# Optimization experiments

Hardware: AMD Instinct MI355X
Metric: run time of the kernel (lower is better)

Reference implementation:

```python
import jax, jax.numpy as jnp
import numpy as np

T, B, N, F = 128, 8, 32, 128
H = 256  # hidden channels
DEG = 8


def setup_inputs() -> dict:
    key = jax.random.key(0)
    ks = jax.random.split(key, 8)
    data = jax.random.normal(ks[0], (T, B, N, F), jnp.float32)
    all_ohs = jax.random.normal(ks[1], (T, B, N, 8), jnp.float32)
    n0 = B * N * T
    n1 = B * N * (T // 2)
    edge_index0 = jax.random.randint(ks[2], (2, n0 * DEG), 0, n0)
    edge_index1 = jax.random.randint(ks[3], (2, n1 * DEG), 0, n1)
    def init(k, shape, fan):
        return jax.random.normal(k, shape, jnp.float32) / np.float32(np.sqrt(fan))
    W0 = init(ks[4], (2 * F, H), 2 * F); b0 = jnp.zeros((H,), jnp.float32)
    Wc0 = init(ks[5], (H, H, 5), H * 5); bc0 = jnp.zeros((H,), jnp.float32)
    W1 = init(ks[6], (2 * H, H), 2 * H); b1 = jnp.zeros((H,), jnp.float32)
    Wc1 = init(ks[7], (H, H, 5), H * 5); bc1 = jnp.zeros((H,), jnp.float32)
    return dict(data=data, all_ohs=all_ohs,
                edge_index0=edge_index0, edge_index1=edge_index1,
                W0=W0, b0=b0, Wc0=Wc0, bc0=bc0,
                W1=W1, b1=b1, Wc1=Wc1, bc1=bc1)


def edge_conv(x, edge_index, W, b):
    # PyG EdgeConv: out_i = max_{(j->i)} relu(Linear(cat[x_i, x_j - x_i]))
    src, dst = edge_index[0], edge_index[1]
    x_i = x[dst]           # [E, C] target features
    x_j = x[src]           # [E, C] source features
    msg = jax.nn.relu(jnp.concatenate([x_i, x_j - x_i], axis=-1) @ W + b)
    out = jax.ops.segment_max(msg, dst, num_segments=x.shape[0])
    return jnp.where(jnp.isneginf(out), 0.0, out)  # empty segments -> 0 (PyG fill)


def temp_conv(x, Wc, bc):
    # x: [BN, C, L]; Conv1d(k=5, pad=2) + relu + MaxPool1d(2)
    y = jax.lax.conv_general_dilated(x, Wc, (1,), [(2, 2)],
                                     dimension_numbers=('NCH', 'OIH', 'NCH'))
    y = jax.nn.relu(y + bc[None, :, None])
    L2 = y.shape[-1] // 2
    y = y[..., : L2 * 2].reshape(y.shape[0], y.shape[1], L2, 2)
    return jnp.max(y, axis=-1)


def reference(data, all_ohs, edge_index0, edge_index1,
              W0, b0, Wc0, bc0, W1, b1, Wc1, bc1):
    # 'fast' path, context=False: all_ohs unused beyond reshape
    length = data.shape[0]
    x = data.reshape(T, B * N, F).transpose(1, 0, 2).reshape(-1, F)  # [BN*T, F]
    layers = ((edge_index0, W0, b0, Wc0, bc0),
              (edge_index1, W1, b1, Wc1, bc1))
    for ei, W, b, Wc, bc in layers:
        x = edge_conv(x, ei, W, b)                       # [BN*length, C]
        x = x.reshape(-1, length, x.shape[-1])           # [BN, length, C]
        x = x.transpose(0, 2, 1)                         # [BN, C, length]
        x = temp_conv(x, Wc, bc)                         # [BN, C, length//2]
        length = x.shape[2]
        C = x.shape[1]
        x = x.transpose(0, 2, 1).reshape(-1, C)          # [BN*length, C]
    return x
```

## Files before the change

### kernel.cpp

```cpp
#include <hip/hip_runtime.h>
#include <hip/hip_bf16.h>
#include <math.h>

#define T0 128
#define BN 256
#define Ff 128
#define Hh 256
#define NODE0 32768
#define E0 262144
#define T1 64
#define NODE1 16384
#define E1 131072
#define CAP 48

typedef __attribute__((ext_vector_type(8))) short bhalf8;
typedef __attribute__((ext_vector_type(4))) float floatx4;

__device__ __forceinline__ unsigned short f2bf(float x) {
  union { float f; unsigned u; } v; v.f = x;
  unsigned r = v.u + 0x7fff + ((v.u >> 16) & 1);
  return (unsigned short)(r >> 16);
}
__device__ __forceinline__ float bf2f(unsigned short b) {
  union { unsigned u; float f; } v; v.u = ((unsigned)b) << 16;
  return v.f;
}


__global__ void k_permb(const float* __restrict__ src, unsigned short* __restrict__ dst) {
  int idx = blockIdx.x * 256 + threadIdx.x;
  int c8 = idx & 15;
  int r  = idx >> 4;
  int t  = r & (T0 - 1);
  int bn = r >> 7;
  const float* s = src + ((size_t)t * BN + bn) * Ff + c8 * 8;
  float4 a = *(const float4*)s;
  float4 b = *(const float4*)(s + 4);
  unsigned short o[8];
  o[0] = f2bf(a.x); o[1] = f2bf(a.y); o[2] = f2bf(a.z); o[3] = f2bf(a.w);
  o[4] = f2bf(b.x); o[5] = f2bf(b.y); o[6] = f2bf(b.z); o[7] = f2bf(b.w);
  *(int4*)(dst + ((size_t)(bn * T0 + t) * Ff + c8 * 8)) = *(int4*)o;
}

__global__ void k_wb(const float* __restrict__ W, unsigned short* __restrict__ Wbot_b,
                     unsigned short* __restrict__ Wd_b, int half, int kbits) {
  int idx = blockIdx.x * 256 + threadIdx.x;
  int n = idx >> kbits;
  int k = idx & (half - 1);
  float top = W[(size_t)k * 256 + n];
  float bot = W[(size_t)(half + k) * 256 + n];
  Wbot_b[idx] = f2bf(bot);
  Wd_b[idx]   = f2bf(top - bot);
}

__global__ void k_wtb(const float* __restrict__ Wc, unsigned short* __restrict__ Wtb) {
  int idx = blockIdx.x * 256 + threadIdx.x;
  int tap = idx >> 16;
  int o = (idx >> 8) & 255;
  int i = idx & 255;
  Wtb[idx] = f2bf(Wc[((size_t)o * 256 + i) * 5 + tap]);
}


__global__ void k_fill(const int* __restrict__ srcIdx, const int* __restrict__ dstIdx,
                       int* __restrict__ cnt, int* __restrict__ slot, int E) {
  int e = blockIdx.x * 256 + threadIdx.x;
  if (e < E) {
    int d = dstIdx[e];
    int p = atomicAdd(&cnt[d], 1);
    if (p < CAP) slot[(size_t)d * CAP + p] = srcIdx[e];
  }
}

__global__ __launch_bounds__(256) void k_maxg(const unsigned short* __restrict__ Bm,
                                              const int* __restrict__ cnt,
                                              const int* __restrict__ slot,
                                              unsigned short* __restrict__ Mm) {
  int node = blockIdx.x * 4 + (threadIdx.x >> 6);
  int lane = threadIdx.x & 63;
  int n = cnt[node];
  if (n > CAP) n = CAP;
  const int* sl = slot + (size_t)node * CAP;
  float4 m = make_float4(-INFINITY, -INFINITY, -INFINITY, -INFINITY);
  int i = 0;
  for (; i + 4 <= n; i += 4) {
    int s0 = sl[i], s1 = sl[i + 1], s2 = sl[i + 2], s3 = sl[i + 3];
    ushort4 v0 = *(const ushort4*)(Bm + (size_t)s0 * 256 + lane * 4);
    ushort4 v1 = *(const ushort4*)(Bm + (size_t)s1 * 256 + lane * 4);
    ushort4 v2 = *(const ushort4*)(Bm + (size_t)s2 * 256 + lane * 4);
    ushort4 v3 = *(const ushort4*)(Bm + (size_t)s3 * 256 + lane * 4);
    m.x = fmaxf(fmaxf(fmaxf(m.x, bf2f(v0.x)), fmaxf(bf2f(v1.x), bf2f(v2.x))), bf2f(v3.x));
    m.y = fmaxf(fmaxf(fmaxf(m.y, bf2f(v0.y)), fmaxf(bf2f(v1.y), bf2f(v2.y))), bf2f(v3.y));
    m.z = fmaxf(fmaxf(fmaxf(m.z, bf2f(v0.z)), fmaxf(bf2f(v1.z), bf2f(v2.z))), bf2f(v3.z));
    m.w = fmaxf(fmaxf(fmaxf(m.w, bf2f(v0.w)), fmaxf(bf2f(v1.w), bf2f(v2.w))), bf2f(v3.w));
  }
  for (; i < n; ++i) {
    int s = sl[i];
    ushort4 v = *(const ushort4*)(Bm + (size_t)s * 256 + lane * 4);
    m.x = fmaxf(m.x, bf2f(v.x));
    m.y = fmaxf(m.y, bf2f(v.y));
    m.z = fmaxf(m.z, bf2f(v.z));
    m.w = fmaxf(m.w, bf2f(v.w));
  }
  ushort4 o;
  o.x = f2bf(m.x); o.y = f2bf(m.y); o.z = f2bf(m.z); o.w = f2bf(m.w);
  *(ushort4*)(Mm + (size_t)node * 256 + lane * 4) = o;
}

template <int MODE>
__global__ __launch_bounds__(256) void k_gemm(const unsigned short* __restrict__ A,
                                              const unsigned short* __restrict__ Wb,
                                              unsigned short* __restrict__ C, int K,
                                              const float* __restrict__ bias,
                                              const unsigned short* __restrict__ Mm) {
  __shared__ __align__(16) short A_lds[128 * 72];
  __shared__ __align__(16) short B_lds[128 * 72];
  int tid = threadIdx.x;
  int row0 = blockIdx.x * 128;
  int col0 = blockIdx.y * 128;
  int lane = tid & 63, wv = tid >> 6;
  int m16 = lane & 15, quad = lane >> 4;

  floatx4 acc[2][8];
#pragma unroll
  for (int mt = 0; mt < 2; ++mt)
#pragma unroll
    for (int nt = 0; nt < 8; ++nt) acc[mt][nt] = (floatx4){0.f, 0.f, 0.f, 0.f};

  for (int kb = 0; kb < K; kb += 64) {
    __syncthreads();
#pragma unroll
    for (int i = 0; i < 4; ++i) {
      int u = tid + i * 256;
      int r = u >> 3, seg = u & 7;
      *(int4*)&A_lds[r * 72 + seg * 8] =
          *(const int4*)(A + (size_t)(row0 + r) * K + kb + seg * 8);
      *(int4*)&B_lds[r * 72 + seg * 8] =
          *(const int4*)(Wb + (size_t)(col0 + r) * K + kb + seg * 8);
    }
    __syncthreads();
#pragma unroll
    for (int ks = 0; ks < 2; ++ks) {
      bhalf8 a[2];
#pragma unroll
      for (int mt = 0; mt < 2; ++mt)
        a[mt] = *(const bhalf8*)&A_lds[(wv * 32 + mt * 16 + m16) * 72 + ks * 32 + quad * 8];
#pragma unroll
      for (int nt = 0; nt < 8; ++nt) {
        bhalf8 b = *(const bhalf8*)&B_lds[(nt * 16 + m16) * 72 + ks * 32 + quad * 8];
#pragma unroll
        for (int mt = 0; mt < 2; ++mt)
          acc[mt][nt] = __builtin_amdgcn_mfma_f32_16x16x32_bf16(a[mt], b, acc[mt][nt], 0, 0, 0);
      }
    }
  }

#pragma unroll
  for (int mt = 0; mt < 2; ++mt) {
    int g0 = row0 + wv * 32 + mt * 16 + quad * 4;
#pragma unroll
    for (int nt = 0; nt < 8; ++nt) {
      int c = col0 + nt * 16 + m16;
      float bv = (MODE == 1) ? bias[c] : 0.f;
#pragma unroll
      for (int r = 0; r < 4; ++r) {
        float v = acc[mt][nt][r];
        if (MODE == 1) v = fmaxf(v + bv + bf2f(Mm[(size_t)(g0 + r) * 256 + c]), 0.f);
        C[(size_t)(g0 + r) * 256 + c] = f2bf(v);
      }
    }
  }
}

template <int TR, bool OUT_F32>
__global__ __launch_bounds__(256) void k_conv(const unsigned short* __restrict__ X,
                                              const unsigned short* __restrict__ Wtb,
                                              const float* __restrict__ bc,
                                              void* __restrict__ Yout) {
  const int MT = TR / 64;
  __shared__ __align__(16) short A_lds[(TR + 4) * 72];
  __shared__ __align__(16) short B_lds[128 * 72];
  int tid = threadIdx.x;
  int row0 = blockIdx.x * TR;
  int col0 = blockIdx.y * 128;
  int lane = tid & 63, wv = tid >> 6;
  int m16 = lane & 15, quad = lane >> 4;

  floatx4 acc[MT][8];
#pragma unroll
  for (int mt = 0; mt < MT; ++mt)
#pragma unroll
    for (int nt = 0; nt < 8; ++nt) acc[mt][nt] = (floatx4){0.f, 0.f, 0.f, 0.f};

  for (int kb = 0; kb < 256; kb += 64) {
    __syncthreads();
    for (int u = tid; u < (TR + 4) * 8; u += 256) {
      int r = u >> 3, seg = u & 7;
      int tt = r - 2;
      int4 v = {0, 0, 0, 0};
      if (tt >= 0 && tt < TR)
        v = *(const int4*)(X + (size_t)(row0 + tt) * 256 + kb + seg * 8);
      *(int4*)&A_lds[r * 72 + seg * 8] = v;
    }
    for (int tap = 0; tap < 5; ++tap) {
      if (tap > 0) __syncthreads();
      const unsigned short* Wk = Wtb + (size_t)tap * 65536;
#pragma unroll
      for (int i = 0; i < 4; ++i) {
        int u = tid + i * 256;
        int r = u >> 3, seg = u & 7;
        *(int4*)&B_lds[r * 72 + seg * 8] =
            *(const int4*)(Wk + (size_t)(col0 + r) * 256 + kb + seg * 8);
      }
      __syncthreads();
#pragma unroll
      for (int ks = 0; ks < 2; ++ks) {
        bhalf8 a[MT];
#pragma unroll
        for (int mt = 0; mt < MT; ++mt)
          a[mt] = *(const bhalf8*)&A_lds[(wv * (16 * MT) + mt * 16 + m16 + tap) * 72 + ks * 32 + quad * 8];
#pragma unroll
        for (int nt = 0; nt < 8; ++nt) {
          bhalf8 b = *(const bhalf8*)&B_lds[(nt * 16 + m16) * 72 + ks * 32 + quad * 8];
#pragma unroll
          for (int mt = 0; mt < MT; ++mt)
            acc[mt][nt] = __builtin_amdgcn_mfma_f32_16x16x32_bf16(a[mt], b, acc[mt][nt], 0, 0, 0);
        }
      }
    }
  }

#pragma unroll
  for (int mt = 0; mt < MT; ++mt) {
    int gbase = row0 + wv * (16 * MT) + mt * 16 + quad * 4;
#pragma unroll
    for (int nt = 0; nt < 8; ++nt) {
      int c = col0 + nt * 16 + m16;
      float bv = bc[c];
      float y0 = fmaxf(acc[mt][nt][0] + bv, 0.f);
      float y1 = fmaxf(acc[mt][nt][1] + bv, 0.f);
      float y2 = fmaxf(acc[mt][nt][2] + bv, 0.f);
      float y3 = fmaxf(acc[mt][nt][3] + bv, 0.f);
      float p0 = fmaxf(y0, y1);
      float p1 = fmaxf(y2, y3);
      int o0 = gbase >> 1;
      if (OUT_F32) {
        float* Y = (float*)Yout;
        Y[(size_t)o0 * 256 + c] = p0;
        Y[(size_t)(o0 + 1) * 256 + c] = p1;
      } else {
        unsigned short* Y = (unsigned short*)Yout;
        Y[(size_t)o0 * 256 + c] = f2bf(p0);
        Y[(size_t)(o0 + 1) * 256 + c] = f2bf(p1);
      }
    }
  }
}

extern "C" void kernel_launch(void* const* d_in, const int* in_sizes, int n_in,
                              void* d_out, int out_size, void* d_ws, size_t ws_size,
                              hipStream_t stream) {
  const float* data = (const float*)d_in[0];
  const int* ei0 = (const int*)d_in[2];
  const int* ei1 = (const int*)d_in[3];
  const float* W0  = (const float*)d_in[4];
  const float* b0  = (const float*)d_in[5];
  const float* Wc0 = (const float*)d_in[6];
  const float* bc0 = (const float*)d_in[7];
  const float* W1  = (const float*)d_in[8];
  const float* b1  = (const float*)d_in[9];
  const float* Wc1 = (const float*)d_in[10];
  const float* bc1 = (const float*)d_in[11];
  float* out = (float*)d_out;

  char* base = (char*)d_ws;
  size_t off = 0;
  auto alloc = [&](size_t bytes) { void* p = base + off; off += (bytes + 255) & ~(size_t)255; return p; };
  unsigned short* X0b   = (unsigned short*)alloc((size_t)NODE0 * Ff * 2);
  unsigned short* Bm    = (unsigned short*)alloc((size_t)NODE0 * Hh * 2);
  unsigned short* Mm    = (unsigned short*)alloc((size_t)NODE0 * Hh * 2);
  unsigned short* X1b   = (unsigned short*)alloc((size_t)NODE0 * Hh * 2);
  unsigned short* Y0b   = (unsigned short*)alloc((size_t)NODE1 * Hh * 2);
  unsigned short* Wbot0 = (unsigned short*)alloc(256 * 128 * 2);
  unsigned short* Wd0   = (unsigned short*)alloc(256 * 128 * 2);
  unsigned short* Wbot1 = (unsigned short*)alloc(256 * 256 * 2);
  unsigned short* Wd1   = (unsigned short*)alloc(256 * 256 * 2);
  unsigned short* Wtb0  = (unsigned short*)alloc(5 * 65536 * 2);
  unsigned short* Wtb1  = (unsigned short*)alloc(5 * 65536 * 2);
  int* cnt0  = (int*)alloc(NODE0 * 4);
  int* cnt1  = (int*)alloc(NODE1 * 4);
  int* slot0 = (int*)alloc((size_t)NODE0 * CAP * 4);
  int* slot1 = (int*)alloc((size_t)NODE1 * CAP * 4);

  hipMemsetAsync(cnt0, 0, NODE0 * sizeof(int), stream);
  hipMemsetAsync(cnt1, 0, NODE1 * sizeof(int), stream);

  k_permb<<<NODE0 * 16 / 256, 256, 0, stream>>>(data, X0b);
  k_wb<<<256 * 128 / 256, 256, 0, stream>>>(W0, Wbot0, Wd0, 128, 7);
  k_wb<<<256 * 256 / 256, 256, 0, stream>>>(W1, Wbot1, Wd1, 256, 8);
  k_wtb<<<5 * 65536 / 256, 256, 0, stream>>>(Wc0, Wtb0);
  k_wtb<<<5 * 65536 / 256, 256, 0, stream>>>(Wc1, Wtb1);

  k_fill<<<E0 / 256, 256, 0, stream>>>(ei0, ei0 + E0, cnt0, slot0, E0);
  k_gemm<0><<<dim3(NODE0 / 128, 2), 256, 0, stream>>>(X0b, Wbot0, Bm, 128, nullptr, nullptr);
  k_maxg<<<NODE0 / 4, 256, 0, stream>>>(Bm, cnt0, slot0, Mm);
  k_gemm<1><<<dim3(NODE0 / 128, 2), 256, 0, stream>>>(X0b, Wd0, X1b, 128, b0, Mm);
  k_conv<128, false><<<dim3(BN, 2), 256, 0, stream>>>(X1b, Wtb0, bc0, Y0b);

  k_fill<<<E1 / 256, 256, 0, stream>>>(ei1, ei1 + E1, cnt1, slot1, E1);
  k_gemm<0><<<dim3(NODE1 / 128, 2), 256, 0, stream>>>(Y0b, Wbot1, Bm, 256, nullptr, nullptr);
  k_maxg<<<NODE1 / 4, 256, 0, stream>>>(Bm, cnt1, slot1, Mm);
  k_gemm<1><<<dim3(NODE1 / 128, 2), 256, 0, stream>>>(Y0b, Wd1, X1b, 256, b1, Mm);
  k_conv<64, true><<<dim3(BN, 2), 256, 0, stream>>>(X1b, Wtb1, bc1, out);
}
```

Measured before the change: 265.0 us.

## Register-prefetch next K tiles in gemm/conv and merge prep kernels into one launch

The GEMM and temporal-conv kernels now load the next K-slice (and the next conv tap's weights) from global memory into registers while the MFMAs on the current LDS tile run, then write them to LDS between two barriers. The conv loop is flattened into 20 tap-by-K steps, and its halo rows are zeroed once up front. Separately, the five prep kernels are merged into one block-indexed k_prep launch and the two counter memsets into one, relying on cnt0 and cnt1 being adjacent in the workspace. This aims to hide global load latency and cut launch overhead, at the cost of more registers per thread and a dependency on the allocation layout.

Measured after the change: 338.9 us. +27.9%, slower.

```diff
diff --git a/kernel.cpp b/kernel.cpp
--- a/kernel.cpp
+++ b/kernel.cpp
@@ -26,39 +26,51 @@
   return v.f;
 }
 
-
-__global__ void k_permb(const float* __restrict__ src, unsigned short* __restrict__ dst) {
-  int idx = blockIdx.x * 256 + threadIdx.x;
-  int c8 = idx & 15;
-  int r  = idx >> 4;
-  int t  = r & (T0 - 1);
-  int bn = r >> 7;
-  const float* s = src + ((size_t)t * BN + bn) * Ff + c8 * 8;
-  float4 a = *(const float4*)s;
-  float4 b = *(const float4*)(s + 4);
-  unsigned short o[8];
-  o[0] = f2bf(a.x); o[1] = f2bf(a.y); o[2] = f2bf(a.z); o[3] = f2bf(a.w);
-  o[4] = f2bf(b.x); o[5] = f2bf(b.y); o[6] = f2bf(b.z); o[7] = f2bf(b.w);
-  *(int4*)(dst + ((size_t)(bn * T0 + t) * Ff + c8 * 8)) = *(int4*)o;
-}
-
-__global__ void k_wb(const float* __restrict__ W, unsigned short* __restrict__ Wbot_b,
-                     unsigned short* __restrict__ Wd_b, int half, int kbits) {
-  int idx = blockIdx.x * 256 + threadIdx.x;
-  int n = idx >> kbits;
-  int k = idx & (half - 1);
-  float top = W[(size_t)k * 256 + n];
-  float bot = W[(size_t)(half + k) * 256 + n];
-  Wbot_b[idx] = f2bf(bot);
-  Wd_b[idx]   = f2bf(top - bot);
-}
-
-__global__ void k_wtb(const float* __restrict__ Wc, unsigned short* __restrict__ Wtb) {
-  int idx = blockIdx.x * 256 + threadIdx.x;
-  int tap = idx >> 16;
-  int o = (idx >> 8) & 255;
-  int i = idx & 255;
-  Wtb[idx] = f2bf(Wc[((size_t)o * 256 + i) * 5 + tap]);
+__global__ void k_prep(const float* __restrict__ data, unsigned short* __restrict__ X0b,
+                       const float* __restrict__ W0, unsigned short* __restrict__ Wbot0,
+                       unsigned short* __restrict__ Wd0,
+                       const float* __restrict__ W1, unsigned short* __restrict__ Wbot1,
+                       unsigned short* __restrict__ Wd1,
+                       const float* __restrict__ Wc0, unsigned short* __restrict__ Wtb0,
+                       const float* __restrict__ Wc1, unsigned short* __restrict__ Wtb1) {
+  int b = blockIdx.x;
+  int tid = threadIdx.x;
+  if (b < 2048) {
+    int idx = b * 256 + tid;
+    int c8 = idx & 15;
+    int r  = idx >> 4;
+    int t  = r & (T0 - 1);
+    int bn = r >> 7;
+    const float* s = data + ((size_t)t * BN + bn) * Ff + c8 * 8;
+    float4 a = *(const float4*)s;
+    float4 bb = *(const float4*)(s + 4);
+    unsigned short o[8];
+    o[0] = f2bf(a.x); o[1] = f2bf(a.y); o[2] = f2bf(a.z); o[3] = f2bf(a.w);
+    o[4] = f2bf(bb.x); o[5] = f2bf(bb.y); o[6] = f2bf(bb.z); o[7] = f2bf(bb.w);
+    *(int4*)(X0b + ((size_t)(bn * T0 + t) * Ff + c8 * 8)) = *(int4*)o;
+  } else if (b < 2176) {
+    int idx = (b - 2048) * 256 + tid;
+    int n = idx >> 7, k = idx & 127;
+    float top = W0[(size_t)k * 256 + n];
+    float bot = W0[(size_t)(128 + k) * 256 + n];
+    Wbot0[idx] = f2bf(bot);
+    Wd0[idx]   = f2bf(top - bot);
+  } else if (b < 2432) {
+    int idx = (b - 2176) * 256 + tid;
+    int n = idx >> 8, k = idx & 255;
+    float top = W1[(size_t)k * 256 + n];
+    float bot = W1[(size_t)(256 + k) * 256 + n];
+    Wbot1[idx] = f2bf(bot);
+    Wd1[idx]   = f2bf(top - bot);
+  } else if (b < 3712) {
+    int idx = (b - 2432) * 256 + tid;
+    int tap = idx >> 16, o = (idx >> 8) & 255, i = idx & 255;
+    Wtb0[idx] = f2bf(Wc0[((size_t)o * 256 + i) * 5 + tap]);
+  } else {
+    int idx = (b - 3712) * 256 + tid;
+    int tap = idx >> 16, o = (idx >> 8) & 255, i = idx & 255;
+    Wtb1[idx] = f2bf(Wc1[((size_t)o * 256 + i) * 5 + tap]);
+  }
 }
 
 
@@ -120,6 +132,22 @@
   int col0 = blockIdx.y * 128;
   int lane = tid & 63, wv = tid >> 6;
   int m16 = lane & 15, quad = lane >> 4;
+  int sr = tid >> 3, sseg = tid & 7;
+
+  int4 Ar[4], Br[4];
+#pragma unroll
+  for (int i = 0; i < 4; ++i) {
+    int r = sr + i * 32;
+    Ar[i] = *(const int4*)(A + (size_t)(row0 + r) * K + sseg * 8);
+    Br[i] = *(const int4*)(Wb + (size_t)(col0 + r) * K + sseg * 8);
+  }
+#pragma unroll
+  for (int i = 0; i < 4; ++i) {
+    int r = sr + i * 32;
+    *(int4*)&A_lds[r * 72 + sseg * 8] = Ar[i];
+    *(int4*)&B_lds[r * 72 + sseg * 8] = Br[i];
+  }
+  __syncthreads();
 
   floatx4 acc[2][8];
 #pragma unroll
@@ -127,18 +155,17 @@
 #pragma unroll
     for (int nt = 0; nt < 8; ++nt) acc[mt][nt] = (floatx4){0.f, 0.f, 0.f, 0.f};
 
-  for (int kb = 0; kb < K; kb += 64) {
-    __syncthreads();
-#pragma unroll
-    for (int i = 0; i < 4; ++i) {
-      int u = tid + i * 256;
-      int r = u >> 3, seg = u & 7;
-      *(int4*)&A_lds[r * 72 + seg * 8] =
-          *(const int4*)(A + (size_t)(row0 + r) * K + kb + seg * 8);
-      *(int4*)&B_lds[r * 72 + seg * 8] =
-          *(const int4*)(Wb + (size_t)(col0 + r) * K + kb + seg * 8);
-    }
-    __syncthreads();
+  int NKB = K >> 6;
+  for (int s = 0; s < NKB; ++s) {
+    if (s + 1 < NKB) {
+      int kb = (s + 1) << 6;
+#pragma unroll
+      for (int i = 0; i < 4; ++i) {
+        int r = sr + i * 32;
+        Ar[i] = *(const int4*)(A + (size_t)(row0 + r) * K + kb + sseg * 8);
+        Br[i] = *(const int4*)(Wb + (size_t)(col0 + r) * K + kb + sseg * 8);
+      }
+    }
 #pragma unroll
     for (int ks = 0; ks < 2; ++ks) {
       bhalf8 a[2];
@@ -152,6 +179,16 @@
         for (int mt = 0; mt < 2; ++mt)
           acc[mt][nt] = __builtin_amdgcn_mfma_f32_16x16x32_bf16(a[mt], b, acc[mt][nt], 0, 0, 0);
       }
+    }
+    if (s + 1 < NKB) {
+      __syncthreads();
+#pragma unroll
+      for (int i = 0; i < 4; ++i) {
+        int r = sr + i * 32;
+        *(int4*)&A_lds[r * 72 + sseg * 8] = Ar[i];
+        *(int4*)&B_lds[r * 72 + sseg * 8] = Br[i];
+      }
+      __syncthreads();
     }
   }
 
@@ -178,6 +215,8 @@
                                               const float* __restrict__ bc,
                                               void* __restrict__ Yout) {
   const int MT = TR / 64;
+  const int AN = TR / 32;
+  const int NS = 20;
   __shared__ __align__(16) short A_lds[(TR + 4) * 72];
   __shared__ __align__(16) short B_lds[128 * 72];
   int tid = threadIdx.x;
@@ -185,6 +224,28 @@
   int col0 = blockIdx.y * 128;
   int lane = tid & 63, wv = tid >> 6;
   int m16 = lane & 15, quad = lane >> 4;
+  int sr = tid >> 3, sseg = tid & 7;
+
+  if (tid < 32) {
+    int r = tid >> 3;
+    int rr = (r < 2) ? r : (TR + r);
+    *(int4*)&A_lds[rr * 72 + (tid & 7) * 8] = (int4){0, 0, 0, 0};
+  }
+
+  int4 Ar[AN], Br[4];
+#pragma unroll
+  for (int i = 0; i < AN; ++i)
+    Ar[i] = *(const int4*)(X + (size_t)(row0 + sr + i * 32) * 256 + sseg * 8);
+#pragma unroll
+  for (int i = 0; i < 4; ++i)
+    Br[i] = *(const int4*)(Wtb + (size_t)(col0 + sr + i * 32) * 256 + sseg * 8);
+#pragma unroll
+  for (int i = 0; i < AN; ++i)
+    *(int4*)&A_lds[(sr + i * 32 + 2) * 72 + sseg * 8] = Ar[i];
+#pragma unroll
+  for (int i = 0; i < 4; ++i)
+    *(int4*)&B_lds[(sr + i * 32) * 72 + sseg * 8] = Br[i];
+  __syncthreads();
 
   floatx4 acc[MT][8];
 #pragma unroll
@@ -192,41 +253,50 @@
 #pragma unroll
     for (int nt = 0; nt < 8; ++nt) acc[mt][nt] = (floatx4){0.f, 0.f, 0.f, 0.f};
 
-  for (int kb = 0; kb < 256; kb += 64) {
-    __syncthreads();
-    for (int u = tid; u < (TR + 4) * 8; u += 256) {
-      int r = u >> 3, seg = u & 7;
-      int tt = r - 2;
-      int4 v = {0, 0, 0, 0};
-      if (tt >= 0 && tt < TR)
-        v = *(const int4*)(X + (size_t)(row0 + tt) * 256 + kb + seg * 8);
-      *(int4*)&A_lds[r * 72 + seg * 8] = v;
-    }
-    for (int tap = 0; tap < 5; ++tap) {
-      if (tap > 0) __syncthreads();
-      const unsigned short* Wk = Wtb + (size_t)tap * 65536;
-#pragma unroll
-      for (int i = 0; i < 4; ++i) {
-        int u = tid + i * 256;
-        int r = u >> 3, seg = u & 7;
-        *(int4*)&B_lds[r * 72 + seg * 8] =
-            *(const int4*)(Wk + (size_t)(col0 + r) * 256 + kb + seg * 8);
-      }
+#pragma unroll 5
+  for (int s = 0; s < NS; ++s) {
+    int sn = s + 1;
+    int tap_n = sn % 5;
+    int kb_n = (sn / 5) << 6;
+    bool hn = sn < NS;
+    if (hn) {
+#pragma unroll
+      for (int i = 0; i < 4; ++i)
+        Br[i] = *(const int4*)(Wtb + (size_t)tap_n * 65536 +
+                               (size_t)(col0 + sr + i * 32) * 256 + kb_n + sseg * 8);
+      if (tap_n == 0) {
+#pragma unroll
+        for (int i = 0; i < AN; ++i)
+          Ar[i] = *(const int4*)(X + (size_t)(row0 + sr + i * 32) * 256 + kb_n + sseg * 8);
+      }
+    }
+    int tap = s % 5;
+#pragma unroll
+    for (int ks = 0; ks < 2; ++ks) {
+      bhalf8 a[MT];
+#pragma unroll
+      for (int mt = 0; mt < MT; ++mt)
+        a[mt] = *(const bhalf8*)&A_lds[(wv * (16 * MT) + mt * 16 + m16 + tap) * 72 +
+                                       ks * 32 + quad * 8];
+#pragma unroll
+      for (int nt = 0; nt < 8; ++nt) {
+        bhalf8 b = *(const bhalf8*)&B_lds[(nt * 16 + m16) * 72 + ks * 32 + quad * 8];
+#pragma unroll
+        for (int mt = 0; mt < MT; ++mt)
+          acc[mt][nt] = __builtin_amdgcn_mfma_f32_16x16x32_bf16(a[mt], b, acc[mt][nt], 0, 0, 0);
+      }
+    }
+    if (hn) {
       __syncthreads();
 #pragma unroll
-      for (int ks = 0; ks < 2; ++ks) {
-        bhalf8 a[MT];
-#pragma unroll
-        for (int mt = 0; mt < MT; ++mt)
-          a[mt] = *(const bhalf8*)&A_lds[(wv * (16 * MT) + mt * 16 + m16 + tap) * 72 + ks * 32 + quad * 8];
-#pragma unroll
-        for (int nt = 0; nt < 8; ++nt) {
-          bhalf8 b = *(const bhalf8*)&B_lds[(nt * 16 + m16) * 72 + ks * 32 + quad * 8];
-#pragma unroll
-          for (int mt = 0; mt < MT; ++mt)
-            acc[mt][nt] = __builtin_amdgcn_mfma_f32_16x16x32_bf16(a[mt], b, acc[mt][nt], 0, 0, 0);
-        }
-      }
+      for (int i = 0; i < 4; ++i)
+        *(int4*)&B_lds[(sr + i * 32) * 72 + sseg * 8] = Br[i];
+      if (tap_n == 0) {
+#pragma unroll
+        for (int i = 0; i < AN; ++i)
+          *(int4*)&A_lds[(sr + i * 32 + 2) * 72 + sseg * 8] = Ar[i];
+      }
+      __syncthreads();
     }
   }
 
@@ -291,15 +361,12 @@
   int* cnt1  = (int*)alloc(NODE1 * 4);
   int* slot0 = (int*)alloc((size_t)NODE0 * CAP * 4);
   int* slot1 = (int*)alloc((size_t)NODE1 * CAP * 4);
-
-  hipMemsetAsync(cnt0, 0, NODE0 * sizeof(int), stream);
-  hipMemsetAsync(cnt1, 0, NODE1 * sizeof(int), stream);
-
-  k_permb<<<NODE0 * 16 / 256, 256, 0, stream>>>(data, X0b);
-  k_wb<<<256 * 128 / 256, 256, 0, stream>>>(W0, Wbot0, Wd0, 128, 7);
-  k_wb<<<256 * 256 / 256, 256, 0, stream>>>(W1, Wbot1, Wd1, 256, 8);
-  k_wtb<<<5 * 65536 / 256, 256, 0, stream>>>(Wc0, Wtb0);
-  k_wtb<<<5 * 65536 / 256, 256, 0, stream>>>(Wc1, Wtb1);
+  (void)cnt1;
+
+  hipMemsetAsync(cnt0, 0, (NODE0 + NODE1) * sizeof(int), stream);
+
+  k_prep<<<4992, 256, 0, stream>>>(data, X0b, W0, Wbot0, Wd0, W1, Wbot1, Wd1,
+                                   Wc0, Wtb0, Wc1, Wtb1);
 
   k_fill<<<E0 / 256, 256, 0, stream>>>(ei0, ei0 + E0, cnt0, slot0, E0);
   k_gemm<0><<<dim3(NODE0 / 128, 2), 256, 0, stream>>>(X0b, Wbot0, Bm, 128, nullptr, nullptr);
```
